# Kernel tuning notes

Hardware: AMD Instinct MI355X
Metric: run time of the kernel (lower is better)

Reference implementation:

```python
import jax, jax.numpy as jnp
import numpy as np
import math

D = 512      # d_model = sd_dim*2
DFF = 512    # dim_feedforward
S = 512      # num_seg (queries)
T = 32768    # video frames (keys)
RATE = 4     # self-attention band half-width
SCALE = 1.0 / math.sqrt(D)


def _ln(x, g, b):
    m = x.mean(-1, keepdims=True)
    v = ((x - m) ** 2).mean(-1, keepdims=True)
    return (x - m) / jnp.sqrt(v + 1e-5) * g + b


def setup_inputs() -> dict:
    key = jax.random.key(0)
    ks = jax.random.split(key, 12)
    w = lambda k, shp, s=0.02: jax.random.normal(k, shp, jnp.float32) * s
    # exactly S contiguous action segments over T frames
    action_idx = jnp.asarray((np.arange(T) * S) // T, dtype=jnp.int32)
    return dict(
        tgt=w(ks[0], (S, 1, D), 1.0), memory=w(ks[1], (T, 1, D), 1.0),
        pos=w(ks[2], (T, 1, D), 0.1), query_pos=w(ks[3], (S, 1, D), 0.1),
        action_idx=action_idx,
        ca_t2l_w=w(ks[4], (D, D)), ca_t2l_b=jnp.zeros(D),
        ca_l1_w=w(ks[5], (DFF, D)), ca_l1_b=jnp.zeros(DFF),
        ca_l2_w=w(ks[6], (D, DFF)), ca_l2_b=jnp.zeros(D),
        ca_n2_g=jnp.ones(D), ca_n2_b=jnp.zeros(D),
        ca_n3_g=jnp.ones(D), ca_n3_b=jnp.zeros(D),
        sa_conv_w=w(ks[7], (D, D)), sa_conv_b=jnp.zeros(D),
        sa_l1_w=w(ks[8], (DFF, D)), sa_l1_b=jnp.zeros(DFF),
        sa_l2_w=w(ks[9], (D, DFF)), sa_l2_b=jnp.zeros(D),
        sa_n1_g=jnp.ones(D), sa_n1_b=jnp.zeros(D),
        sa_n2_g=jnp.ones(D), sa_n2_b=jnp.zeros(D),
    )


def reference(tgt, memory, pos, query_pos, action_idx,
              ca_t2l_w, ca_t2l_b, ca_l1_w, ca_l1_b, ca_l2_w, ca_l2_b,
              ca_n2_g, ca_n2_b, ca_n3_g, ca_n3_b,
              sa_conv_w, sa_conv_b, sa_l1_w, sa_l1_b, sa_l2_w, sa_l2_b,
              sa_n1_g, sa_n1_b, sa_n2_g, sa_n2_b):
    # ---------------- CrossAttention (segment mask) ----------------
    q = tgt + query_pos                      # (S,1,D)
    k = memory + pos                         # (T,1,D)
    scores = jnp.einsum('sbd,tbd->bst', q, k) * SCALE   # (1,S,T)
    # segment id per frame from change points of action_idx
    chg = (action_idx[1:] != action_idx[:-1]).astype(jnp.int32)
    seg_id = jnp.concatenate([jnp.zeros(1, jnp.int32), jnp.cumsum(chg)])  # (T,)
    # query i attends to segments i-1, i, i+1
    mask = jnp.abs(seg_id[None, :] - jnp.arange(S, dtype=jnp.int32)[:, None]) <= 1  # (S,T)
    scores = jnp.where(mask[None], scores, -jnp.inf)
    attn = jax.nn.softmax(scores, axis=-1)               # (1,S,T)
    tgt2 = jnp.einsum('bst,tbd->sbd', attn, memory)      # (S,1,D)
    tgt2 = jnp.maximum(tgt2, 0.0) @ ca_t2l_w.T + ca_t2l_b
    x = _ln(tgt + tgt2, ca_n2_g, ca_n2_b)
    ffn = jnp.maximum(x @ ca_l1_w.T + ca_l1_b, 0.0) @ ca_l2_w.T + ca_l2_b
    x = _ln(x + ffn, ca_n3_g, ca_n3_b)                   # (S,1,D)
    # ---------------- SelfAttention (banded, pos=None) ----------------
    src = jnp.transpose(x, (1, 0, 2))                    # (1,S,D)
    s2 = jnp.einsum('bsd,btd->bst', src, src) * SCALE    # (1,S,S)
    i = jnp.arange(S)
    band = jnp.abs(i[:, None] - i[None, :]) <= RATE      # (S,S)
    s2 = jnp.where(band[None], s2, -jnp.inf)
    a2 = jax.nn.softmax(s2, axis=-1)                     # (1,S,S)
    src2 = jnp.einsum('bqk,bkd->bqd', a2, src)           # (1,S,D)
    src2 = jnp.maximum(src2, 0.0) @ sa_conv_w.T + sa_conv_b  # 1x1 conv over channels
    y = _ln(src + src2, sa_n1_g, sa_n1_b)
    ffn2 = jnp.maximum(y @ sa_l1_w.T + sa_l1_b, 0.0) @ sa_l2_w.T + sa_l2_b
    y = _ln(y + ffn2, sa_n2_g, sa_n2_b)
    return y                                              # (1,S,D)
```

## Files before the change

kernel.cpp:

```cpp
#include <hip/hip_runtime.h>

#define S_Q 512
#define DIM 512
#define SCALE_F 0.04419417382415922f
#define LDS_W 520

typedef short short8 __attribute__((ext_vector_type(8)));
typedef float floatx4 __attribute__((ext_vector_type(4)));

__device__ __forceinline__ float wave_sum(float v) {
#pragma unroll
  for (int o = 32; o > 0; o >>= 1) v += __shfl_xor(v, o);
  return v;
}
__device__ __forceinline__ unsigned short f2bf(float f) {
  unsigned u = __float_as_uint(f);
  return (unsigned short)((u + 0x7FFFu + ((u >> 16) & 1u)) >> 16);
}
__device__ __forceinline__ float bf2f(short s) {
  return __uint_as_float(((unsigned)(unsigned short)s) << 16);
}

__global__ __launch_bounds__(256) void k_ca_partial(
    const float* __restrict__ tgt, const float* __restrict__ qpos,
    const float* __restrict__ mem, const float* __restrict__ pos,
    unsigned short* __restrict__ part_acc, float* __restrict__ part_ms) {
  const int j = blockIdx.x;
  const int tid = threadIdx.x;
  const int wave = tid >> 6, lane = tid & 63;
  const int d0 = lane * 8;
  __shared__ float wacc[4][3][DIM];
  __shared__ float wms[4][3][2];

  float qf[3][8];
#pragma unroll
  for (int c = 0; c < 3; ++c) {
    const int qi = j - 1 + c;
    if ((unsigned)qi < (unsigned)S_Q) {
      float4 t0 = *(const float4*)(tgt + (size_t)qi * DIM + d0);
      float4 t1 = *(const float4*)(tgt + (size_t)qi * DIM + d0 + 4);
      float4 q0 = *(const float4*)(qpos + (size_t)qi * DIM + d0);
      float4 q1 = *(const float4*)(qpos + (size_t)qi * DIM + d0 + 4);
      qf[c][0] = t0.x + q0.x; qf[c][1] = t0.y + q0.y;
      qf[c][2] = t0.z + q0.z; qf[c][3] = t0.w + q0.w;
      qf[c][4] = t1.x + q1.x; qf[c][5] = t1.y + q1.y;
      qf[c][6] = t1.z + q1.z; qf[c][7] = t1.w + q1.w;
    } else {
#pragma unroll
      for (int e = 0; e < 8; ++e) qf[c][e] = 0.f;
    }
  }

  float m[3] = {-1e30f, -1e30f, -1e30f};
  float ssum[3] = {0.f, 0.f, 0.f};
  float acc[3][8];
#pragma unroll
  for (int c = 0; c < 3; ++c)
#pragma unroll
    for (int e = 0; e < 8; ++e) acc[c][e] = 0.f;

  const float* mbase = mem + ((size_t)j * 64 + wave * 16) * DIM + d0;
  const float* pbase = pos + ((size_t)j * 64 + wave * 16) * DIM + d0;

  for (int b = 0; b < 4; ++b) {
    float mv[4][8], kk[4][8];
#pragma unroll
    for (int f = 0; f < 4; ++f) {
      const float* mp = mbase + (size_t)(b * 4 + f) * DIM;
      const float* pp = pbase + (size_t)(b * 4 + f) * DIM;
      float4 a = *(const float4*)mp;
      float4 bb = *(const float4*)(mp + 4);
      float4 c4 = *(const float4*)pp;
      float4 dd = *(const float4*)(pp + 4);
      mv[f][0] = a.x;  mv[f][1] = a.y;  mv[f][2] = a.z;  mv[f][3] = a.w;
      mv[f][4] = bb.x; mv[f][5] = bb.y; mv[f][6] = bb.z; mv[f][7] = bb.w;
      kk[f][0] = a.x + c4.x;  kk[f][1] = a.y + c4.y;
      kk[f][2] = a.z + c4.z;  kk[f][3] = a.w + c4.w;
      kk[f][4] = bb.x + dd.x; kk[f][5] = bb.y + dd.y;
      kk[f][6] = bb.z + dd.z; kk[f][7] = bb.w + dd.w;
    }
    float dots[3][4];
#pragma unroll
    for (int f = 0; f < 4; ++f) {
      float s0 = 0.f, s1 = 0.f, s2 = 0.f;
#pragma unroll
      for (int e = 0; e < 8; ++e) {
        s0 += qf[0][e] * kk[f][e];
        s1 += qf[1][e] * kk[f][e];
        s2 += qf[2][e] * kk[f][e];
      }
      dots[0][f] = s0; dots[1][f] = s1; dots[2][f] = s2;
    }
#pragma unroll
    for (int o = 32; o > 0; o >>= 1)
#pragma unroll
      for (int c = 0; c < 3; ++c)
#pragma unroll
        for (int f = 0; f < 4; ++f) dots[c][f] += __shfl_xor(dots[c][f], o);
#pragma unroll
    for (int c = 0; c < 3; ++c) {
      float s[4];
#pragma unroll
      for (int f = 0; f < 4; ++f) s[f] = dots[c][f] * SCALE_F;
      const float bm = fmaxf(fmaxf(s[0], s[1]), fmaxf(s[2], s[3]));
      const float nm = fmaxf(m[c], bm);
      const float fct = __expf(m[c] - nm);
      m[c] = nm;
      ssum[c] *= fct;
#pragma unroll
      for (int e = 0; e < 8; ++e) acc[c][e] *= fct;
#pragma unroll
      for (int f = 0; f < 4; ++f) {
        const float w = __expf(s[f] - nm);
        ssum[c] += w;
#pragma unroll
        for (int e = 0; e < 8; ++e) acc[c][e] += w * mv[f][e];
      }
    }
  }

#pragma unroll
  for (int c = 0; c < 3; ++c) {
    *(float4*)(&wacc[wave][c][d0]) =
        make_float4(acc[c][0], acc[c][1], acc[c][2], acc[c][3]);
    *(float4*)(&wacc[wave][c][d0 + 4]) =
        make_float4(acc[c][4], acc[c][5], acc[c][6], acc[c][7]);
    if (lane == 0) { wms[wave][c][0] = m[c]; wms[wave][c][1] = ssum[c]; }
  }
  __syncthreads();

  const int d = tid * 2;
#pragma unroll
  for (int c = 0; c < 3; ++c) {
    const int qi = j - 1 + c;
    if ((unsigned)qi >= (unsigned)S_Q) continue;
    float M = wms[0][c][0];
#pragma unroll
    for (int w = 1; w < 4; ++w) M = fmaxf(M, wms[w][c][0]);
    float S = 0.f, ax = 0.f, ay = 0.f;
#pragma unroll
    for (int w = 0; w < 4; ++w) {
      const float wg = __expf(wms[w][c][0] - M);
      S += wg * wms[w][c][1];
      const float2 a = *(const float2*)(&wacc[w][c][d]);
      ax += wg * a.x;
      ay += wg * a.y;
    }
    const size_t slot = (size_t)qi * 3 + c;
    unsigned short* dst = part_acc + slot * DIM + d;
    dst[0] = f2bf(ax);
    dst[1] = f2bf(ay);
    if (tid == 0) {
      part_ms[slot * 2 + 0] = M;
      part_ms[slot * 2 + 1] = S;
    }
  }
}

__device__ __forceinline__ void stage_tile(const float* __restrict__ G,
                                           short* __restrict__ Ls,
                                           int rowblk, int tid) {
  const int w = tid >> 6, lane = tid & 63;
  const int col = lane * 8;
#pragma unroll
  for (int u = 0; u < 8; ++u) {
    const int row = u * 4 + w;
    const float* src = G + (size_t)(rowblk * 32 + row) * DIM + col;
    float4 a = *(const float4*)src;
    float4 b = *(const float4*)(src + 4);
    short8 s;
    s[0] = (short)f2bf(a.x); s[1] = (short)f2bf(a.y);
    s[2] = (short)f2bf(a.z); s[3] = (short)f2bf(a.w);
    s[4] = (short)f2bf(b.x); s[5] = (short)f2bf(b.y);
    s[6] = (short)f2bf(b.z); s[7] = (short)f2bf(b.w);
    *(short8*)(&Ls[row * LDS_W + col]) = s;
  }
}

template <bool RELU>
__device__ __forceinline__ void gemm_core(const short* __restrict__ As,
                                          const short* __restrict__ Ws,
                                          const float* __restrict__ bias,
                                          float* __restrict__ C, int bx, int by,
                                          int wave, int lane) {
  const int r0 = (wave >> 1) * 16, c0 = (wave & 1) * 16;
  const int frow = lane & 15, fk = (lane >> 4) * 8;
  const short* ap = &As[(r0 + frow) * LDS_W + fk];
  const short* wp = &Ws[(c0 + frow) * LDS_W + fk];
  floatx4 acc = {0.f, 0.f, 0.f, 0.f};
#pragma unroll
  for (int kc = 0; kc < 16; ++kc) {
    const short8 af = *(const short8*)(ap + kc * 32);
    const short8 wf = *(const short8*)(wp + kc * 32);
    acc = __builtin_amdgcn_mfma_f32_16x16x32_bf16(af, wf, acc, 0, 0, 0);
  }
  const int col = bx * 32 + c0 + frow;
  const int rowb = by * 32 + r0 + (lane >> 4) * 4;
  const float b = bias[col];
#pragma unroll
  for (int r = 0; r < 4; ++r) {
    float v = acc[r] + b;
    if (RELU) v = fmaxf(v, 0.f);
    C[(size_t)(rowb + r) * DIM + col] = v;
  }
}

__device__ __forceinline__ void ln_prologue(const float* __restrict__ X,
                                            const float* __restrict__ R,
                                            const float* __restrict__ g,
                                            const float* __restrict__ b,
                                            short* __restrict__ As, int by,
                                            float* x_out, int wave, int lane) {
  const int d0 = lane * 8;
  float gg[8], bb[8];
  {
    float4 g0 = *(const float4*)(g + d0);
    float4 g1 = *(const float4*)(g + d0 + 4);
    float4 b0 = *(const float4*)(b + d0);
    float4 b1 = *(const float4*)(b + d0 + 4);
    gg[0] = g0.x; gg[1] = g0.y; gg[2] = g0.z; gg[3] = g0.w;
    gg[4] = g1.x; gg[5] = g1.y; gg[6] = g1.z; gg[7] = g1.w;
    bb[0] = b0.x; bb[1] = b0.y; bb[2] = b0.z; bb[3] = b0.w;
    bb[4] = b1.x; bb[5] = b1.y; bb[6] = b1.z; bb[7] = b1.w;
  }
  for (int r = wave; r < 32; r += 4) {
    const int grow = by * 32 + r;
    const float* xp = X + (size_t)grow * DIM + d0;
    const float* rp = R + (size_t)grow * DIM + d0;
    float4 x0 = *(const float4*)xp;
    float4 x1 = *(const float4*)(xp + 4);
    float4 r0 = *(const float4*)rp;
    float4 r1 = *(const float4*)(rp + 4);
    float v[8] = {x0.x + r0.x, x0.y + r0.y, x0.z + r0.z, x0.w + r0.w,
                  x1.x + r1.x, x1.y + r1.y, x1.z + r1.z, x1.w + r1.w};
    float s = 0.f, sq = 0.f;
#pragma unroll
    for (int e = 0; e < 8; ++e) { s += v[e]; sq += v[e] * v[e]; }
#pragma unroll
    for (int o = 32; o > 0; o >>= 1) {
      s += __shfl_xor(s, o);
      sq += __shfl_xor(sq, o);
    }
    const float mean = s * (1.f / DIM);
    const float var = sq * (1.f / DIM) - mean * mean;
    const float rstd = rsqrtf(var + 1e-5f);
    float o8[8];
    short8 sv;
#pragma unroll
    for (int e = 0; e < 8; ++e) {
      o8[e] = (v[e] - mean) * rstd * gg[e] + bb[e];
      sv[e] = (short)f2bf(o8[e]);
    }
    *(short8*)(&As[r * LDS_W + d0]) = sv;
    if (x_out) {
      *(float4*)(x_out + (size_t)grow * DIM + d0) =
          make_float4(o8[0], o8[1], o8[2], o8[3]);
      *(float4*)(x_out + (size_t)grow * DIM + d0 + 4) =
          make_float4(o8[4], o8[5], o8[6], o8[7]);
    }
  }
}

__global__ __launch_bounds__(256) void k_g1(
    const unsigned short* __restrict__ part_acc,
    const float* __restrict__ part_ms, const float* __restrict__ W,
    const float* __restrict__ bias, float* __restrict__ C) {
  __shared__ short As[32 * LDS_W];
  __shared__ short Ws[32 * LDS_W];
  const int tid = threadIdx.x;
  const int bx = blockIdx.x, by = blockIdx.y;
  const int wave = tid >> 6, lane = tid & 63;
  const int d0 = lane * 8;
  for (int r = wave; r < 32; r += 4) {
    const int i = by * 32 + r;
    const bool valid[3] = {i < S_Q - 1, true, i > 0};
    float mm[3], ss[3], M = -1e30f;
#pragma unroll
    for (int c = 0; c < 3; ++c) {
      if (valid[c]) {
        mm[c] = part_ms[((size_t)i * 3 + c) * 2 + 0];
        ss[c] = part_ms[((size_t)i * 3 + c) * 2 + 1];
        M = fmaxf(M, mm[c]);
      } else {
        mm[c] = -1e30f;
        ss[c] = 0.f;
      }
    }
    float den = 0.f, wg[3];
#pragma unroll
    for (int c = 0; c < 3; ++c) {
      wg[c] = valid[c] ? __expf(mm[c] - M) : 0.f;
      den += wg[c] * ss[c];
    }
    const float inv = 1.f / den;
    float o[8] = {0.f, 0.f, 0.f, 0.f, 0.f, 0.f, 0.f, 0.f};
#pragma unroll
    for (int c = 0; c < 3; ++c) {
      if (valid[c]) {
        const short8 pa =
            *(const short8*)(part_acc + ((size_t)i * 3 + c) * DIM + d0);
#pragma unroll
        for (int e = 0; e < 8; ++e) o[e] += wg[c] * bf2f(pa[e]);
      }
    }
    short8 sv;
#pragma unroll
    for (int e = 0; e < 8; ++e) sv[e] = (short)f2bf(fmaxf(o[e] * inv, 0.f));
    *(short8*)(&As[r * LDS_W + d0]) = sv;
  }
  stage_tile(W, Ws, bx, tid);
  __syncthreads();
  gemm_core<false>(As, Ws, bias, C, bx, by, wave, lane);
}

__global__ __launch_bounds__(256) void k_gln(
    const float* __restrict__ X, const float* __restrict__ R,
    const float* __restrict__ g, const float* __restrict__ b,
    const float* __restrict__ W, const float* __restrict__ bias,
    float* __restrict__ C, float* __restrict__ x_out) {
  __shared__ short As[32 * LDS_W];
  __shared__ short Ws[32 * LDS_W];
  const int tid = threadIdx.x;
  const int bx = blockIdx.x, by = blockIdx.y;
  const int wave = tid >> 6, lane = tid & 63;
  ln_prologue(X, R, g, b, As, by, (bx == 0) ? x_out : nullptr, wave, lane);
  stage_tile(W, Ws, bx, tid);
  __syncthreads();
  gemm_core<true>(As, Ws, bias, C, bx, by, wave, lane);
}

__global__ __launch_bounds__(256) void k_gplain(
    const float* __restrict__ A, const float* __restrict__ W,
    const float* __restrict__ bias, float* __restrict__ C) {
  __shared__ short As[32 * LDS_W];
  __shared__ short Ws[32 * LDS_W];
  const int tid = threadIdx.x;
  const int bx = blockIdx.x, by = blockIdx.y;
  const int wave = tid >> 6, lane = tid & 63;
  stage_tile(A, As, by, tid);
  stage_tile(W, Ws, bx, tid);
  __syncthreads();
  gemm_core<false>(As, Ws, bias, C, bx, by, wave, lane);
}

__global__ __launch_bounds__(256) void k_g4(
    const float* __restrict__ X, const float* __restrict__ R,
    const float* __restrict__ g, const float* __restrict__ b,
    const float* __restrict__ W, const float* __restrict__ bias,
    float* __restrict__ C, float* __restrict__ x2_out) {
  __shared__ short Xw[40 * LDS_W];
  __shared__ short As[32 * LDS_W];
  __shared__ short Ws[32 * LDS_W];
  const int tid = threadIdx.x;
  const int bx = blockIdx.x, by = blockIdx.y;
  const int wave = tid >> 6, lane = tid & 63;
  const int d0 = lane * 8;
  const int wlo = (by * 32 - 4 > 0) ? by * 32 - 4 : 0;
  const int whi = (by * 32 + 35 < S_Q - 1) ? by * 32 + 35 : S_Q - 1;
  const int nw = whi - wlo + 1;

  {
    float gg[8], bb[8];
    float4 g0 = *(const float4*)(g + d0);
    float4 g1 = *(const float4*)(g + d0 + 4);
    float4 b0 = *(const float4*)(b + d0);
    float4 b1 = *(const float4*)(b + d0 + 4);
    gg[0] = g0.x; gg[1] = g0.y; gg[2] = g0.z; gg[3] = g0.w;
    gg[4] = g1.x; gg[5] = g1.y; gg[6] = g1.z; gg[7] = g1.w;
    bb[0] = b0.x; bb[1] = b0.y; bb[2] = b0.z; bb[3] = b0.w;
    bb[4] = b1.x; bb[5] = b1.y; bb[6] = b1.z; bb[7] = b1.w;
    for (int r = wave; r < nw; r += 4) {
      const int grow = wlo + r;
      const float* xp = X + (size_t)grow * DIM + d0;
      const float* rp = R + (size_t)grow * DIM + d0;
      float4 x0 = *(const float4*)xp;
      float4 x1 = *(const float4*)(xp + 4);
      float4 r0 = *(const float4*)rp;
      float4 r1 = *(const float4*)(rp + 4);
      float v[8] = {x0.x + r0.x, x0.y + r0.y, x0.z + r0.z, x0.w + r0.w,
                    x1.x + r1.x, x1.y + r1.y, x1.z + r1.z, x1.w + r1.w};
      float s = 0.f, sq = 0.f;
#pragma unroll
      for (int e = 0; e < 8; ++e) { s += v[e]; sq += v[e] * v[e]; }
#pragma unroll
      for (int o = 32; o > 0; o >>= 1) {
        s += __shfl_xor(s, o);
        sq += __shfl_xor(sq, o);
      }
      const float mean = s * (1.f / DIM);
      const float var = sq * (1.f / DIM) - mean * mean;
      const float rstd = rsqrtf(var + 1e-5f);
      float o8[8];
      short8 sv;
#pragma unroll
      for (int e = 0; e < 8; ++e) {
        o8[e] = (v[e] - mean) * rstd * gg[e] + bb[e];
        sv[e] = (short)f2bf(o8[e]);
      }
      *(short8*)(&Xw[r * LDS_W + d0]) = sv;
      if (bx == 0 && grow >= by * 32 && grow < by * 32 + 32) {
        *(float4*)(x2_out + (size_t)grow * DIM + d0) =
            make_float4(o8[0], o8[1], o8[2], o8[3]);
        *(float4*)(x2_out + (size_t)grow * DIM + d0 + 4) =
            make_float4(o8[4], o8[5], o8[6], o8[7]);
      }
    }
  }
  stage_tile(W, Ws, bx, tid);
  __syncthreads();

  for (int li = wave; li < 32; li += 4) {
    const int i = by * 32 + li;
    const int lq = i - wlo;
    float qv[8];
    {
      const short8 qs = *(const short8*)(&Xw[lq * LDS_W + d0]);
#pragma unroll
      for (int e = 0; e < 8; ++e) qv[e] = bf2f(qs[e]);
    }
    const int jlo = (i - 4 > 0) ? i - 4 : 0;
    const int jhi = (i + 4 < S_Q - 1) ? i + 4 : S_Q - 1;
    const int n = jhi - jlo + 1;
    float sc[9];
#pragma unroll
    for (int k = 0; k < 9; ++k) {
      if (k < n) {
        const int lk = jlo + k - wlo;
        const short8 ks = *(const short8*)(&Xw[lk * LDS_W + d0]);
        float dd = 0.f;
#pragma unroll
        for (int e = 0; e < 8; ++e) dd += qv[e] * bf2f(ks[e]);
        sc[k] = dd;
      } else {
        sc[k] = 0.f;
      }
    }
#pragma unroll
    for (int o = 32; o > 0; o >>= 1)
#pragma unroll
      for (int k = 0; k < 9; ++k) sc[k] += __shfl_xor(sc[k], o);
    float M = -1e30f;
#pragma unroll
    for (int k = 0; k < 9; ++k) {
      sc[k] *= SCALE_F;
      if (k < n) M = fmaxf(M, sc[k]);
    }
    float p[9], den = 0.f;
#pragma unroll
    for (int k = 0; k < 9; ++k) {
      p[k] = (k < n) ? __expf(sc[k] - M) : 0.f;
      den += p[k];
    }
    const float inv = 1.f / den;
    float o8[8] = {0.f, 0.f, 0.f, 0.f, 0.f, 0.f, 0.f, 0.f};
#pragma unroll
    for (int k = 0; k < 9; ++k) {
      if (k < n) {
        const int lk = jlo + k - wlo;
        const short8 ks = *(const short8*)(&Xw[lk * LDS_W + d0]);
#pragma unroll
        for (int e = 0; e < 8; ++e) o8[e] += p[k] * bf2f(ks[e]);
      }
    }
    short8 sv;
#pragma unroll
    for (int e = 0; e < 8; ++e) sv[e] = (short)f2bf(fmaxf(o8[e] * inv, 0.f));
    *(short8*)(&As[li * LDS_W + d0]) = sv;
  }
  __syncthreads();
  gemm_core<false>(As, Ws, bias, C, bx, by, wave, lane);
}

__global__ __launch_bounds__(256) void k_addln(
    const float* __restrict__ X, const float* __restrict__ R,
    const float* __restrict__ g, const float* __restrict__ b,
    float* __restrict__ out) {
  const int row = blockIdx.x * 4 + (threadIdx.x >> 6);
  const int lane = threadIdx.x & 63;
  const int d = lane * 8;
  const float4* xp = (const float4*)(X + (size_t)row * DIM + d);
  const float4* rp = (const float4*)(R + (size_t)row * DIM + d);
  float4 x0 = xp[0], x1 = xp[1], r0 = rp[0], r1 = rp[1];
  float v[8] = {x0.x + r0.x, x0.y + r0.y, x0.z + r0.z, x0.w + r0.w,
                x1.x + r1.x, x1.y + r1.y, x1.z + r1.z, x1.w + r1.w};
  float s = 0.f, sq = 0.f;
#pragma unroll
  for (int e = 0; e < 8; ++e) { s += v[e]; sq += v[e] * v[e]; }
  s = wave_sum(s);
  sq = wave_sum(sq);
  const float mean = s * (1.f / DIM);
  const float var = sq * (1.f / DIM) - mean * mean;
  const float rstd = rsqrtf(var + 1e-5f);
  const float4* gp = (const float4*)(g + d);
  const float4* bp = (const float4*)(b + d);
  float4 g0 = gp[0], g1 = gp[1], bb0 = bp[0], bb1 = bp[1];
  float4 o0, o1;
  o0.x = (v[0] - mean) * rstd * g0.x + bb0.x;
  o0.y = (v[1] - mean) * rstd * g0.y + bb0.y;
  o0.z = (v[2] - mean) * rstd * g0.z + bb0.z;
  o0.w = (v[3] - mean) * rstd * g0.w + bb0.w;
  o1.x = (v[4] - mean) * rstd * g1.x + bb1.x;
  o1.y = (v[5] - mean) * rstd * g1.y + bb1.y;
  o1.z = (v[6] - mean) * rstd * g1.z + bb1.z;
  o1.w = (v[7] - mean) * rstd * g1.w + bb1.w;
  *(float4*)(out + (size_t)row * DIM + d) = o0;
  *(float4*)(out + (size_t)row * DIM + d + 4) = o1;
}

extern "C" void kernel_launch(void* const* d_in, const int* in_sizes, int n_in,
                              void* d_out, int out_size, void* d_ws, size_t ws_size,
                              hipStream_t stream) {
  const float* tgt       = (const float*)d_in[0];
  const float* memory    = (const float*)d_in[1];
  const float* pos       = (const float*)d_in[2];
  const float* qpos      = (const float*)d_in[3];
  const float* ca_t2l_w  = (const float*)d_in[5];
  const float* ca_t2l_b  = (const float*)d_in[6];
  const float* ca_l1_w   = (const float*)d_in[7];
  const float* ca_l1_b   = (const float*)d_in[8];
  const float* ca_l2_w   = (const float*)d_in[9];
  const float* ca_l2_b   = (const float*)d_in[10];
  const float* ca_n2_g   = (const float*)d_in[11];
  const float* ca_n2_b   = (const float*)d_in[12];
  const float* ca_n3_g   = (const float*)d_in[13];
  const float* ca_n3_b   = (const float*)d_in[14];
  const float* sa_conv_w = (const float*)d_in[15];
  const float* sa_conv_b = (const float*)d_in[16];
  const float* sa_l1_w   = (const float*)d_in[17];
  const float* sa_l1_b   = (const float*)d_in[18];
  const float* sa_l2_w   = (const float*)d_in[19];
  const float* sa_l2_b   = (const float*)d_in[20];
  const float* sa_n1_g   = (const float*)d_in[21];
  const float* sa_n1_b   = (const float*)d_in[22];
  const float* sa_n2_g   = (const float*)d_in[23];
  const float* sa_n2_b   = (const float*)d_in[24];
  float* out = (float*)d_out;
  float* ws = (float*)d_ws;

  unsigned short* part_acc = (unsigned short*)ws;
  float* part_ms = ws + 393216;
  float* t2 = ws + 396288;
  float* h  = ws + 658432;
  float* x  = ws + 920576;
  float* f  = ws + 0;
  float* x2 = ws + 396288;
  float* c  = ws + 658432;
  float* y1 = ws + 0;
  float* h2 = ws + 920576;
  float* f2 = ws + 396288;

  const dim3 gg(16, 16, 1);

  k_ca_partial<<<512, 256, 0, stream>>>(tgt, qpos, memory, pos, part_acc, part_ms);
  k_g1<<<gg, 256, 0, stream>>>(part_acc, part_ms, ca_t2l_w, ca_t2l_b, t2);
  k_gln<<<gg, 256, 0, stream>>>(tgt, t2, ca_n2_g, ca_n2_b, ca_l1_w, ca_l1_b, h, x);
  k_gplain<<<gg, 256, 0, stream>>>(h, ca_l2_w, ca_l2_b, f);
  k_g4<<<gg, 256, 0, stream>>>(x, f, ca_n3_g, ca_n3_b, sa_conv_w, sa_conv_b, c, x2);
  k_gln<<<gg, 256, 0, stream>>>(x2, c, sa_n1_g, sa_n1_b, sa_l1_w, sa_l1_b, h2, y1);
  k_gplain<<<gg, 256, 0, stream>>>(h2, sa_l2_w, sa_l2_b, f2);
  k_addln<<<128, 256, 0, stream>>>(f2, y1, sa_n2_g, sa_n2_b, out);
}
```

Baseline: 281.2 us.

## Rewrite segment cross-attention with bf16 MFMA scores and split each segment in two blocks

The cross-attention partial kernel now stages each half-segment of 32 memory frames as bf16 K and V tiles in LDS. It computes the 3x32 query-key scores with 16x16x32 bf16 MFMA instructions instead of scalar dot products and wave shuffles. The grid doubles to 1024 blocks, each producing per-half partial softmax statistics, and the merge kernel now combines six partials per query instead of three. This cuts the shuffle-reduction and FMA cost of the score stage and adds parallelism, at the cost of bf16 rounding of q and k, a larger workspace, and wasted MFMA rows since only 3 of 16 query rows are valid.

```diff
diff --git a/kernel.cpp b/kernel.cpp
--- a/kernel.cpp
+++ b/kernel.cpp
@@ -4,15 +4,11 @@
 #define DIM 512
 #define SCALE_F 0.04419417382415922f
 #define LDS_W 520
+#define KP 520
 
 typedef short short8 __attribute__((ext_vector_type(8)));
 typedef float floatx4 __attribute__((ext_vector_type(4)));
 
-__device__ __forceinline__ float wave_sum(float v) {
-#pragma unroll
-  for (int o = 32; o > 0; o >>= 1) v += __shfl_xor(v, o);
-  return v;
-}
 __device__ __forceinline__ unsigned short f2bf(float f) {
   unsigned u = __float_as_uint(f);
   return (unsigned short)((u + 0x7FFFu + ((u >> 16) & 1u)) >> 16);
@@ -21,138 +17,131 @@
   return __uint_as_float(((unsigned)(unsigned short)s) << 16);
 }
 
-__global__ __launch_bounds__(256) void k_ca_partial(
+__global__ __launch_bounds__(256) void k_ca_flash(
     const float* __restrict__ tgt, const float* __restrict__ qpos,
     const float* __restrict__ mem, const float* __restrict__ pos,
     unsigned short* __restrict__ part_acc, float* __restrict__ part_ms) {
-  const int j = blockIdx.x;
+  __shared__ short Kt[32 * KP];
+  __shared__ short Vt[32 * KP];
+  __shared__ float scP[4][3][16];
+  __shared__ float sc2[3][32];
+
+  const int b = blockIdx.x;
+  const int j = b >> 1, h = b & 1;
   const int tid = threadIdx.x;
   const int wave = tid >> 6, lane = tid & 63;
-  const int d0 = lane * 8;
-  __shared__ float wacc[4][3][DIM];
-  __shared__ float wms[4][3][2];
-
-  float qf[3][8];
+  const int F0 = j * 64 + h * 32;
+
+#pragma unroll
+  for (int p8 = 0; p8 < 8; ++p8) {
+    const int r = p8 * 4 + wave;
+    const float* mrow = mem + (size_t)(F0 + r) * DIM + lane * 8;
+    const float* prow = pos + (size_t)(F0 + r) * DIM + lane * 8;
+    float4 m0 = *(const float4*)mrow;
+    float4 m1 = *(const float4*)(mrow + 4);
+    float4 p0 = *(const float4*)prow;
+    float4 p1 = *(const float4*)(prow + 4);
+    short8 kk, vv;
+    vv[0] = (short)f2bf(m0.x); vv[1] = (short)f2bf(m0.y);
+    vv[2] = (short)f2bf(m0.z); vv[3] = (short)f2bf(m0.w);
+    vv[4] = (short)f2bf(m1.x); vv[5] = (short)f2bf(m1.y);
+    vv[6] = (short)f2bf(m1.z); vv[7] = (short)f2bf(m1.w);
+    kk[0] = (short)f2bf(m0.x + p0.x); kk[1] = (short)f2bf(m0.y + p0.y);
+    kk[2] = (short)f2bf(m0.z + p0.z); kk[3] = (short)f2bf(m0.w + p0.w);
+    kk[4] = (short)f2bf(m1.x + p1.x); kk[5] = (short)f2bf(m1.y + p1.y);
+    kk[6] = (short)f2bf(m1.z + p1.z); kk[7] = (short)f2bf(m1.w + p1.w);
+    *(short8*)(&Kt[r * KP + lane * 8]) = kk;
+    *(short8*)(&Vt[r * KP + lane * 8]) = vv;
+  }
+
+  const int qrow = lane & 15;
+  const int quad = lane >> 4;
+  const int kbase = (wave >> 1) * 256;
+  const int ntile = wave & 1;
+  const int qi_frag = j - 1 + qrow;
+  const bool qv = (qrow < 3) && ((unsigned)qi_frag < (unsigned)S_Q);
+  short8 afrag[8];
+#pragma unroll
+  for (int t = 0; t < 8; ++t) {
+    if (qv) {
+      const float* tb = tgt + (size_t)qi_frag * DIM + kbase + t * 32 + quad * 8;
+      const float* qb = qpos + (size_t)qi_frag * DIM + kbase + t * 32 + quad * 8;
+      float4 a0 = *(const float4*)tb;
+      float4 a1 = *(const float4*)(tb + 4);
+      float4 b0 = *(const float4*)qb;
+      float4 b1 = *(const float4*)(qb + 4);
+      afrag[t][0] = (short)f2bf(a0.x + b0.x);
+      afrag[t][1] = (short)f2bf(a0.y + b0.y);
+      afrag[t][2] = (short)f2bf(a0.z + b0.z);
+      afrag[t][3] = (short)f2bf(a0.w + b0.w);
+      afrag[t][4] = (short)f2bf(a1.x + b1.x);
+      afrag[t][5] = (short)f2bf(a1.y + b1.y);
+      afrag[t][6] = (short)f2bf(a1.z + b1.z);
+      afrag[t][7] = (short)f2bf(a1.w + b1.w);
+    } else {
+#pragma unroll
+      for (int e = 0; e < 8; ++e) afrag[t][e] = 0;
+    }
+  }
+  __syncthreads();
+
+  floatx4 acc = {0.f, 0.f, 0.f, 0.f};
+  const int frow = ntile * 16 + (lane & 15);
+#pragma unroll
+  for (int t = 0; t < 8; ++t) {
+    const short8 bfrag =
+        *(const short8*)(&Kt[frow * KP + kbase + t * 32 + quad * 8]);
+    acc = __builtin_amdgcn_mfma_f32_16x16x32_bf16(afrag[t], bfrag, acc, 0, 0, 0);
+  }
+  if (quad == 0) {
+#pragma unroll
+    for (int r = 0; r < 3; ++r) scP[wave][r][lane & 15] = acc[r];
+  }
+  __syncthreads();
+
+  if (tid < 96) {
+    const int c = tid >> 5, f = tid & 31;
+    sc2[c][f] = (scP[f >> 4][c][f & 15] + scP[2 + (f >> 4)][c][f & 15]) * SCALE_F;
+  }
+  __syncthreads();
+
+  float m[3];
 #pragma unroll
   for (int c = 0; c < 3; ++c) {
-    const int qi = j - 1 + c;
-    if ((unsigned)qi < (unsigned)S_Q) {
-      float4 t0 = *(const float4*)(tgt + (size_t)qi * DIM + d0);
-      float4 t1 = *(const float4*)(tgt + (size_t)qi * DIM + d0 + 4);
-      float4 q0 = *(const float4*)(qpos + (size_t)qi * DIM + d0);
-      float4 q1 = *(const float4*)(qpos + (size_t)qi * DIM + d0 + 4);
-      qf[c][0] = t0.x + q0.x; qf[c][1] = t0.y + q0.y;
-      qf[c][2] = t0.z + q0.z; qf[c][3] = t0.w + q0.w;
-      qf[c][4] = t1.x + q1.x; qf[c][5] = t1.y + q1.y;
-      qf[c][6] = t1.z + q1.z; qf[c][7] = t1.w + q1.w;
-    } else {
-#pragma unroll
-      for (int e = 0; e < 8; ++e) qf[c][e] = 0.f;
-    }
-  }
-
-  float m[3] = {-1e30f, -1e30f, -1e30f};
-  float ssum[3] = {0.f, 0.f, 0.f};
-  float acc[3][8];
-#pragma unroll
-  for (int c = 0; c < 3; ++c)
-#pragma unroll
-    for (int e = 0; e < 8; ++e) acc[c][e] = 0.f;
-
-  const float* mbase = mem + ((size_t)j * 64 + wave * 16) * DIM + d0;
-  const float* pbase = pos + ((size_t)j * 64 + wave * 16) * DIM + d0;
-
-  for (int b = 0; b < 4; ++b) {
-    float mv[4][8], kk[4][8];
-#pragma unroll
-    for (int f = 0; f < 4; ++f) {
-      const float* mp = mbase + (size_t)(b * 4 + f) * DIM;
-      const float* pp = pbase + (size_t)(b * 4 + f) * DIM;
-      float4 a = *(const float4*)mp;
-      float4 bb = *(const float4*)(mp + 4);
-      float4 c4 = *(const float4*)pp;
-      float4 dd = *(const float4*)(pp + 4);
-      mv[f][0] = a.x;  mv[f][1] = a.y;  mv[f][2] = a.z;  mv[f][3] = a.w;
-      mv[f][4] = bb.x; mv[f][5] = bb.y; mv[f][6] = bb.z; mv[f][7] = bb.w;
-      kk[f][0] = a.x + c4.x;  kk[f][1] = a.y + c4.y;
-      kk[f][2] = a.z + c4.z;  kk[f][3] = a.w + c4.w;
-      kk[f][4] = bb.x + dd.x; kk[f][5] = bb.y + dd.y;
-      kk[f][6] = bb.z + dd.z; kk[f][7] = bb.w + dd.w;
-    }
-    float dots[3][4];
-#pragma unroll
-    for (int f = 0; f < 4; ++f) {
-      float s0 = 0.f, s1 = 0.f, s2 = 0.f;
-#pragma unroll
-      for (int e = 0; e < 8; ++e) {
-        s0 += qf[0][e] * kk[f][e];
-        s1 += qf[1][e] * kk[f][e];
-        s2 += qf[2][e] * kk[f][e];
-      }
-      dots[0][f] = s0; dots[1][f] = s1; dots[2][f] = s2;
-    }
-#pragma unroll
-    for (int o = 32; o > 0; o >>= 1)
-#pragma unroll
-      for (int c = 0; c < 3; ++c)
-#pragma unroll
-        for (int f = 0; f < 4; ++f) dots[c][f] += __shfl_xor(dots[c][f], o);
+    float mm = sc2[c][0];
+#pragma unroll
+    for (int f = 1; f < 32; ++f) mm = fmaxf(mm, sc2[c][f]);
+    m[c] = mm;
+  }
+
+  const int dcol = wave * 128 + lane * 2;
+  float ss[3] = {0.f, 0.f, 0.f};
+  float o0[3] = {0.f, 0.f, 0.f};
+  float o1[3] = {0.f, 0.f, 0.f};
+  for (int f = 0; f < 32; ++f) {
+    const unsigned vv = *(const unsigned*)(&Vt[f * KP + dcol]);
+    const float v0 = bf2f((short)(vv & 0xFFFFu));
+    const float v1 = bf2f((short)(vv >> 16));
 #pragma unroll
     for (int c = 0; c < 3; ++c) {
-      float s[4];
-#pragma unroll
-      for (int f = 0; f < 4; ++f) s[f] = dots[c][f] * SCALE_F;
-      const float bm = fmaxf(fmaxf(s[0], s[1]), fmaxf(s[2], s[3]));
-      const float nm = fmaxf(m[c], bm);
-      const float fct = __expf(m[c] - nm);
-      m[c] = nm;
-      ssum[c] *= fct;
-#pragma unroll
-      for (int e = 0; e < 8; ++e) acc[c][e] *= fct;
-#pragma unroll
-      for (int f = 0; f < 4; ++f) {
-        const float w = __expf(s[f] - nm);
-        ssum[c] += w;
-#pragma unroll
-        for (int e = 0; e < 8; ++e) acc[c][e] += w * mv[f][e];
-      }
-    }
-  }
-
-#pragma unroll
-  for (int c = 0; c < 3; ++c) {
-    *(float4*)(&wacc[wave][c][d0]) =
-        make_float4(acc[c][0], acc[c][1], acc[c][2], acc[c][3]);
-    *(float4*)(&wacc[wave][c][d0 + 4]) =
-        make_float4(acc[c][4], acc[c][5], acc[c][6], acc[c][7]);
-    if (lane == 0) { wms[wave][c][0] = m[c]; wms[wave][c][1] = ssum[c]; }
-  }
-  __syncthreads();
-
-  const int d = tid * 2;
+      const float e = __expf(sc2[c][f] - m[c]);
+      ss[c] += e;
+      o0[c] += e * v0;
+      o1[c] += e * v1;
+    }
+  }
+
 #pragma unroll
   for (int c = 0; c < 3; ++c) {
     const int qi = j - 1 + c;
     if ((unsigned)qi >= (unsigned)S_Q) continue;
-    float M = wms[0][c][0];
-#pragma unroll
-    for (int w = 1; w < 4; ++w) M = fmaxf(M, wms[w][c][0]);
-    float S = 0.f, ax = 0.f, ay = 0.f;
-#pragma unroll
-    for (int w = 0; w < 4; ++w) {
-      const float wg = __expf(wms[w][c][0] - M);
-      S += wg * wms[w][c][1];
-      const float2 a = *(const float2*)(&wacc[w][c][d]);
-      ax += wg * a.x;
-      ay += wg * a.y;
-    }
-    const size_t slot = (size_t)qi * 3 + c;
-    unsigned short* dst = part_acc + slot * DIM + d;
-    dst[0] = f2bf(ax);
-    dst[1] = f2bf(ay);
+    const size_t slot = (size_t)qi * 6 + c * 2 + h;
+    const unsigned pack =
+        (unsigned)f2bf(o0[c]) | ((unsigned)f2bf(o1[c]) << 16);
+    *(unsigned*)(part_acc + slot * DIM + dcol) = pack;
     if (tid == 0) {
-      part_ms[slot * 2 + 0] = M;
-      part_ms[slot * 2 + 1] = S;
+      part_ms[slot * 2 + 0] = m[c];
+      part_ms[slot * 2 + 1] = ss[c];
     }
   }
 }
@@ -274,33 +263,33 @@
   for (int r = wave; r < 32; r += 4) {
     const int i = by * 32 + r;
     const bool valid[3] = {i < S_Q - 1, true, i > 0};
-    float mm[3], ss[3], M = -1e30f;
-#pragma unroll
-    for (int c = 0; c < 3; ++c) {
-      if (valid[c]) {
-        mm[c] = part_ms[((size_t)i * 3 + c) * 2 + 0];
-        ss[c] = part_ms[((size_t)i * 3 + c) * 2 + 1];
-        M = fmaxf(M, mm[c]);
+    float mm[6], ss[6], M = -1e30f;
+#pragma unroll
+    for (int k = 0; k < 6; ++k) {
+      if (valid[k >> 1]) {
+        mm[k] = part_ms[((size_t)i * 6 + k) * 2 + 0];
+        ss[k] = part_ms[((size_t)i * 6 + k) * 2 + 1];
+        M = fmaxf(M, mm[k]);
       } else {
-        mm[c] = -1e30f;
-        ss[c] = 0.f;
-      }
-    }
-    float den = 0.f, wg[3];
-#pragma unroll
-    for (int c = 0; c < 3; ++c) {
-      wg[c] = valid[c] ? __expf(mm[c] - M) : 0.f;
-      den += wg[c] * ss[c];
+        mm[k] = -1e30f;
+        ss[k] = 0.f;
+      }
+    }
+    float den = 0.f, wg[6];
+#pragma unroll
+    for (int k = 0; k < 6; ++k) {
+      wg[k] = valid[k >> 1] ? __expf(mm[k] - M) : 0.f;
+      den += wg[k] * ss[k];
     }
     const float inv = 1.f / den;
     float o[8] = {0.f, 0.f, 0.f, 0.f, 0.f, 0.f, 0.f, 0.f};
 #pragma unroll
-    for (int c = 0; c < 3; ++c) {
-      if (valid[c]) {
+    for (int k = 0; k < 6; ++k) {
+      if (valid[k >> 1]) {
         const short8 pa =
-            *(const short8*)(part_acc + ((size_t)i * 3 + c) * DIM + d0);
-#pragma unroll
-        for (int e = 0; e < 8; ++e) o[e] += wg[c] * bf2f(pa[e]);
+            *(const short8*)(part_acc + ((size_t)i * 6 + k) * DIM + d0);
+#pragma unroll
+        for (int e = 0; e < 8; ++e) o[e] += wg[k] * bf2f(pa[e]);
       }
     }
     short8 sv;
@@ -486,8 +475,11 @@
   float s = 0.f, sq = 0.f;
 #pragma unroll
   for (int e = 0; e < 8; ++e) { s += v[e]; sq += v[e] * v[e]; }
-  s = wave_sum(s);
-  sq = wave_sum(sq);
+#pragma unroll
+  for (int o = 32; o > 0; o >>= 1) {
+    s += __shfl_xor(s, o);
+    sq += __shfl_xor(sq, o);
+  }
   const float mean = s * (1.f / DIM);
   const float var = sq * (1.f / DIM) - mean * mean;
   const float rstd = rsqrtf(var + 1e-5f);
@@ -538,20 +530,20 @@
   float* ws = (float*)d_ws;
 
   unsigned short* part_acc = (unsigned short*)ws;
-  float* part_ms = ws + 393216;
-  float* t2 = ws + 396288;
-  float* h  = ws + 658432;
-  float* x  = ws + 920576;
+  float* part_ms = ws + 786432;
+  float* t2 = ws + 792576;
+  float* h  = ws + 1054720;
+  float* x  = ws + 1316864;
   float* f  = ws + 0;
-  float* x2 = ws + 396288;
-  float* c  = ws + 658432;
+  float* x2 = ws + 792576;
+  float* c  = ws + 1054720;
   float* y1 = ws + 0;
-  float* h2 = ws + 920576;
-  float* f2 = ws + 396288;
+  float* h2 = ws + 1316864;
+  float* f2 = ws + 792576;
 
   const dim3 gg(16, 16, 1);
 
-  k_ca_partial<<<512, 256, 0, stream>>>(tgt, qpos, memory, pos, part_acc, part_ms);
+  k_ca_flash<<<1024, 256, 0, stream>>>(tgt, qpos, memory, pos, part_acc, part_ms);
   k_g1<<<gg, 256, 0, stream>>>(part_acc, part_ms, ca_t2l_w, ca_t2l_b, t2);
   k_gln<<<gg, 256, 0, stream>>>(tgt, t2, ca_n2_g, ca_n2_b, ca_l1_w, ca_l1_b, h, x);
   k_gplain<<<gg, 256, 0, stream>>>(h, ca_l2_w, ca_l2_b, f);
```

Result: slower. 298.3 us (+6.1%).
